# Performance work log

Measured on AMD Instinct MI355X. Metric: run time of the kernel, lower is better.

Reference implementation:

```python
import math
import jax, jax.numpy as jnp
import numpy as np

D_MODEL = 1024
N_HEAD = 16
HEAD_DIM = D_MODEL // N_HEAD
ATTN_MULT = 1.0
# standparam=False (muP): scaling = head_dim**-1 * sqrt(attn_mult)
SCALING = (1.0 / HEAD_DIM) * math.sqrt(ATTN_MULT)
EPS = 1e-5


def layernorm(x, w, b):
    mu = jnp.mean(x, axis=-1, keepdims=True)
    var = jnp.mean(jnp.square(x - mu), axis=-1, keepdims=True)
    return (x - mu) * jax.lax.rsqrt(var + EPS) * w + b


def setup_inputs() -> dict:
    key = jax.random.key(0)
    ks = jax.random.split(key, 6)
    L, N, E = 2048, 2, D_MODEL
    std = 0.02
    return {
        "x": jax.random.normal(ks[0], (L, N, E), jnp.float32),
        "ln1_w": jnp.ones((E,), jnp.float32),
        "ln1_b": jnp.zeros((E,), jnp.float32),
        "in_proj_w": jax.random.normal(ks[1], (3 * E, E), jnp.float32) * std,
        "in_proj_b": jnp.zeros((3 * E,), jnp.float32),
        "out_w": jax.random.normal(ks[2], (E, E), jnp.float32) * std,
        "out_b": jnp.zeros((E,), jnp.float32),
        "ln2_w": jnp.ones((E,), jnp.float32),
        "ln2_b": jnp.zeros((E,), jnp.float32),
        "fc_w": jax.random.normal(ks[3], (4 * E, E), jnp.float32) * std,
        "fc_b": jnp.zeros((4 * E,), jnp.float32),
        "proj_w": jax.random.normal(ks[4], (E, 4 * E), jnp.float32) * std,
        "proj_b": jnp.zeros((E,), jnp.float32),
    }


def block(x, ln1_w, ln1_b, in_proj_w, in_proj_b, out_w, out_b,
          ln2_w, ln2_b, fc_w, fc_b, proj_w, proj_b):
    L, N, E = x.shape
    H, D = N_HEAD, HEAD_DIM
    # --- self-attention on ln_1(x), seq-first layout (L, N, E) ---
    y = layernorm(x, ln1_w, ln1_b)
    qkv = jnp.einsum('lne,fe->lnf', y, in_proj_w) + in_proj_b  # (L, N, 3E)
    q, k, v = jnp.split(qkv, 3, axis=-1)
    q = q * SCALING
    # (L, N, E) -> (N, H, L, D)
    def to_heads(t):
        return t.reshape(L, N, H, D).transpose(1, 2, 0, 3)
    q, k, v = to_heads(q), to_heads(k), to_heads(v)
    scores = jnp.einsum('nhld,nhsd->nhls', q, k)           # (N, H, L, L)
    w = jax.nn.softmax(scores, axis=-1)
    o = jnp.einsum('nhls,nhsd->nhld', w, v)                # (N, H, L, D)
    o = o.transpose(2, 0, 1, 3).reshape(L, N, E)
    attn_out = jnp.einsum('lne,fe->lnf', o, out_w) + out_b
    x = x + attn_out
    # --- MLP on ln_2(x): fc -> GELU -> proj ---
    z = layernorm(x, ln2_w, ln2_b)
    h = jax.nn.gelu(jnp.einsum('lne,fe->lnf', z, fc_w) + fc_b, approximate=False)
    m = jnp.einsum('lnf,ef->lne', h, proj_w) + proj_b
    return x + m


def reference(x, ln1_w, ln1_b, in_proj_w, in_proj_b, out_w, out_b,
              ln2_w, ln2_b, fc_w, fc_b, proj_w, proj_b):
    return block(x, ln1_w, ln1_b, in_proj_w, in_proj_b, out_w, out_b,
                 ln2_w, ln2_b, fc_w, fc_b, proj_w, proj_b)
```

## Files before the change

kernel.cpp:

```cpp
#include <hip/hip_runtime.h>
#include <hip/hip_bf16.h>

typedef unsigned short u16;
typedef float v4f __attribute__((ext_vector_type(4)));
typedef __bf16 v8bf __attribute__((ext_vector_type(8)));
typedef unsigned short v4u __attribute__((ext_vector_type(4)));
typedef unsigned short v8u __attribute__((ext_vector_type(8)));

#define EMB 1024
#define TOK 4096
#define LSEQ 2048
#define NBATCH 2
#define SCALING 0.015625f
#define LN_EPS 1e-5f

__device__ __forceinline__ float bf2f(u16 u) {
  unsigned int i = ((unsigned int)u) << 16;
  return __builtin_bit_cast(float, i);
}
__device__ __forceinline__ u16 f2bf(float f) {
  __hip_bfloat16 h = __float2bfloat16(f);
  return __builtin_bit_cast(u16, h);
}
__device__ __forceinline__ v8bf load8(const u16* p) {
  return *reinterpret_cast<const v8bf*>(p);
}
__device__ __forceinline__ v4f mfma16(v8bf a, v8bf b, v4f c) {
  return __builtin_amdgcn_mfma_f32_16x16x32_bf16(a, b, c, 0, 0, 0);
}
__device__ __forceinline__ void gload16(const u16* g, u16* l) {
  __builtin_amdgcn_global_load_lds(
      (const __attribute__((address_space(1))) void*)g,
      (__attribute__((address_space(3))) void*)l, 16, 0, 0);
}
template <int N>
__device__ __forceinline__ void waitcnt_vm() {
  if constexpr (N == 0) asm volatile("s_waitcnt vmcnt(0)" ::: "memory");
  else if constexpr (N == 2) asm volatile("s_waitcnt vmcnt(2)" ::: "memory");
  else if constexpr (N == 3) asm volatile("s_waitcnt vmcnt(3)" ::: "memory");
  else if constexpr (N == 4) asm volatile("s_waitcnt vmcnt(4)" ::: "memory");
  else if constexpr (N == 6) asm volatile("s_waitcnt vmcnt(6)" ::: "memory");
  else if constexpr (N == 8) asm volatile("s_waitcnt vmcnt(8)" ::: "memory");
}
__device__ __forceinline__ float gelu_fast(float v) {
  float u = v * (0.7978845608f + 0.0356774081f * v * v);
  return v / (1.0f + __expf(-2.0f * u));
}

__global__ __launch_bounds__(256) void cvt_kernel(
    const float* __restrict__ in, u16* __restrict__ out) {
  size_t i = ((size_t)blockIdx.x * 256 + threadIdx.x) * 8;
  v4f a = *reinterpret_cast<const v4f*>(in + i);
  v4f b = *reinterpret_cast<const v4f*>(in + i + 4);
  v8u r;
#pragma unroll
  for (int j = 0; j < 4; j++) { r[j] = f2bf(a[j]); r[4 + j] = f2bf(b[j]); }
  *reinterpret_cast<v8u*>(out + i) = r;
}

__global__ __launch_bounds__(256) void addred_kernel(
    float* __restrict__ out, const u16* __restrict__ p0) {
  size_t i = ((size_t)blockIdx.x * 256 + threadIdx.x) * 8;
  v4f a0 = *reinterpret_cast<const v4f*>(out + i);
  v4f a1 = *reinterpret_cast<const v4f*>(out + i + 4);
  v8u pp = *reinterpret_cast<const v8u*>(p0 + i);
#pragma unroll
  for (int j = 0; j < 4; j++) {
    a0[j] += bf2f(pp[j]);
    a1[j] += bf2f(pp[4 + j]);
  }
  *reinterpret_cast<v4f*>(out + i) = a0;
  *reinterpret_cast<v4f*>(out + i + 4) = a1;
}

template <int MODE>
__global__ __launch_bounds__(256) void ln_kernel(
    const void* __restrict__ xin, const float* __restrict__ w,
    const float* __restrict__ b, u16* __restrict__ y) {
  int t = blockIdx.x, tid = threadIdx.x;
  float v[4];
  if (MODE == 0) {
    v4u raw = *reinterpret_cast<const v4u*>((const u16*)xin + (size_t)t * EMB + tid * 4);
#pragma unroll
    for (int j = 0; j < 4; j++) v[j] = bf2f(raw[j]);
  } else {
    v4f raw = *reinterpret_cast<const v4f*>((const float*)xin + (size_t)t * EMB + tid * 4);
#pragma unroll
    for (int j = 0; j < 4; j++) v[j] = raw[j];
  }
  float s = v[0] + v[1] + v[2] + v[3];
  float ss = v[0] * v[0] + v[1] * v[1] + v[2] * v[2] + v[3] * v[3];
#pragma unroll
  for (int off = 32; off >= 1; off >>= 1) {
    s += __shfl_xor(s, off);
    ss += __shfl_xor(ss, off);
  }
  __shared__ float sm[4], sq[4];
  if ((tid & 63) == 0) { sm[tid >> 6] = s; sq[tid >> 6] = ss; }
  __syncthreads();
  s = sm[0] + sm[1] + sm[2] + sm[3];
  ss = sq[0] + sq[1] + sq[2] + sq[3];
  float mu = s * (1.0f / EMB);
  float var = ss * (1.0f / EMB) - mu * mu;
  float rstd = rsqrtf(var + LN_EPS);
  v4f wv = *reinterpret_cast<const v4f*>(w + tid * 4);
  v4f bv = *reinterpret_cast<const v4f*>(b + tid * 4);
  v4u out;
#pragma unroll
  for (int j = 0; j < 4; j++) out[j] = f2bf((v[j] - mu) * rstd * wv[j] + bv[j]);
  *reinterpret_cast<v4u*>(y + (size_t)t * EMB + tid * 4) = out;
}

template <int BM, int BN>
__global__ __launch_bounds__(256) void gemm_db_kernel(
    const u16* __restrict__ A, const u16* __restrict__ W,
    const float* __restrict__ bias, int K, int Nout, int mode,
    u16* __restrict__ out_bf, float* __restrict__ out_f,
    const float* __restrict__ res_f32, const u16* __restrict__ res_bf) {
  constexpr int NJ = BM * BN / 4096;
  constexpr int CWV = 4 / (BM / 64);
  __shared__ alignas(16) u16 lA[2][BM * 32];
  __shared__ alignas(16) u16 lB[2][BN * 32];

  int tid = threadIdx.x;
  int lane = tid & 63, wid = tid >> 6;
  int quad = lane >> 4, l16 = lane & 15;
  int row0 = blockIdx.x * BM;
  int col0 = blockIdx.y * BN;
  int rw = (wid / CWV) * 64;
  int cw = (wid % CWV) * (BN / CWV);

  v4f zero = {0.f, 0.f, 0.f, 0.f};
  v4f acc[4][NJ];
#pragma unroll
  for (int i = 0; i < 4; i++)
#pragma unroll
    for (int j = 0; j < NJ; j++) acc[i][j] = zero;

  int wbase8 = (tid & 192) * 8;

  auto stage = [&](int buf, int k0) {
    const u16* Ab = A + (size_t)row0 * K + k0;
    const u16* Wb = W + (size_t)col0 * K + k0;
#pragma unroll
    for (int n = 0; n < BM / 64; n++) {
      int slot = n * 256 + tid;
      int seg = slot / BM, r = slot & (BM - 1);
      gload16(Ab + (size_t)r * K + seg * 8, &lA[buf][n * 2048 + wbase8]);
    }
#pragma unroll
    for (int n = 0; n < BN / 64; n++) {
      int slot = n * 256 + tid;
      int seg = slot / BN, r = slot & (BN - 1);
      gload16(Wb + (size_t)r * K + seg * 8, &lB[buf][n * 2048 + wbase8]);
    }
  };

  stage(0, 0);
  int buf = 0;
  for (int k0 = 0; k0 < K; k0 += 32) {
    __syncthreads();
    if (k0 + 32 < K) stage(buf ^ 1, k0 + 32);

    v8bf af[4], bfr[NJ];
#pragma unroll
    for (int i = 0; i < 4; i++)
      af[i] = load8(&lA[buf][(quad * BM + rw + i * 16 + l16) * 8]);
#pragma unroll
    for (int j = 0; j < NJ; j++)
      bfr[j] = load8(&lB[buf][(quad * BN + cw + j * 16 + l16) * 8]);
#pragma unroll
    for (int i = 0; i < 4; i++)
#pragma unroll
      for (int j = 0; j < NJ; j++)
        acc[i][j] = mfma16(af[i], bfr[j], acc[i][j]);
    buf ^= 1;
  }

#pragma unroll
  for (int i = 0; i < 4; i++) {
    int rbase = row0 + rw + i * 16 + quad * 4;
#pragma unroll
    for (int j = 0; j < NJ; j++) {
      int c = col0 + cw + j * 16 + l16;
      float bv = bias[c];
#pragma unroll
      for (int r = 0; r < 4; r++) {
        int tok = rbase + r;
        float v = acc[i][j][r] + bv;
        size_t idx = (size_t)tok * Nout + c;
        if (mode == 1) {
          out_bf[idx] = f2bf(res_f32[idx] + v);
        } else if (mode == 3) {
          out_f[idx] = bf2f(res_bf[idx]) + v;
        }
      }
    }
  }
}

template <int BM, int BN>
__global__ __launch_bounds__(512, 2) void gemm_big_kernel(
    const u16* __restrict__ A, const u16* __restrict__ W,
    const float* __restrict__ bias, int K, int Nout, int mode,
    u16* __restrict__ out_bf, float* __restrict__ out_f,
    const u16* __restrict__ res_bf) {
  constexpr int NI = BM / 32;
  constexpr int NJ = BN / 64;
  constexpr int LOADS = BM / 128 + BN / 128;
  __shared__ alignas(16) u16 lA[3][BM * 32];
  __shared__ alignas(16) u16 lB[3][BN * 32];

  int tid = threadIdx.x;
  int lane = tid & 63, wid = tid >> 6;
  int quad = lane >> 4, l16 = lane & 15;
  int row0 = blockIdx.x * BM;
  int col0 = blockIdx.y * BN;
  int rw = (wid >> 2) * (BM / 2);
  int cw = (wid & 3) * (BN / 4);

  int kbeg = 0, kend = K;
  if (mode == 5) {
    int half = K >> 1;
    kbeg = blockIdx.z * half;
    kend = kbeg + half;
  }
  int nt = (kend - kbeg) >> 5;

  v4f zero = {0.f, 0.f, 0.f, 0.f};
  v4f acc[NI][NJ];
#pragma unroll
  for (int i = 0; i < NI; i++)
#pragma unroll
    for (int j = 0; j < NJ; j++) acc[i][j] = zero;

  int wbase8 = (tid & 448) * 8;

  auto stage = [&](int buf, int k0) {
    const u16* Ab = A + (size_t)row0 * K + k0;
    const u16* Wb = W + (size_t)col0 * K + k0;
#pragma unroll
    for (int n = 0; n < BM / 128; n++) {
      int p = n * 512 + tid;
      int r = p >> 2, sp = p & 3;
      int sl = sp ^ ((r >> 1) & 3);
      gload16(Ab + (size_t)r * K + sl * 8, &lA[buf][n * 4096 + wbase8]);
    }
#pragma unroll
    for (int n = 0; n < BN / 128; n++) {
      int p = n * 512 + tid;
      int r = p >> 2, sp = p & 3;
      int sl = sp ^ ((r >> 1) & 3);
      gload16(Wb + (size_t)r * K + sl * 8, &lB[buf][n * 4096 + wbase8]);
    }
  };

  auto compute = [&](int bidx) {
    v8bf af[NI], bfr[NJ];
#pragma unroll
    for (int i = 0; i < NI; i++) {
      int ra = rw + i * 16 + l16;
      af[i] = load8(&lA[bidx][((ra << 2) + (quad ^ ((ra >> 1) & 3))) << 3]);
    }
#pragma unroll
    for (int j = 0; j < NJ; j++) {
      int rb = cw + j * 16 + l16;
      bfr[j] = load8(&lB[bidx][((rb << 2) + (quad ^ ((rb >> 1) & 3))) << 3]);
    }
#pragma unroll
    for (int i = 0; i < NI; i++)
#pragma unroll
      for (int j = 0; j < NJ; j++)
        acc[i][j] = mfma16(af[i], bfr[j], acc[i][j]);
  };

  stage(0, kbeg);
  stage(1, kbeg + 32);
  for (int t = 0; t < nt - 1; ++t) {
    waitcnt_vm<LOADS>();
    __builtin_amdgcn_s_barrier();
    if (t + 2 < nt) stage((t + 2) % 3, kbeg + (t + 2) * 32);
    compute(t % 3);
  }
  waitcnt_vm<0>();
  __builtin_amdgcn_s_barrier();
  compute((nt - 1) % 3);

#pragma unroll
  for (int i = 0; i < NI; i++) {
    int rbase = row0 + rw + i * 16 + quad * 4;
#pragma unroll
    for (int j = 0; j < NJ; j++) {
      int c = col0 + cw + j * 16 + l16;
      float bv = bias[c];
#pragma unroll
      for (int r = 0; r < 4; r++) {
        int tok = rbase + r;
        float raw = acc[i][j][r];
        float v = raw + bv;
        if (mode == 4) {
          int region = c >> 10;
          int cc = c & 1023;
          int hh = cc >> 6, dd = cc & 63;
          int l = tok >> 1, nn = tok & 1;
          size_t hb = (size_t)(nn * 16 + hh);
          if (region == 0) {
            out_bf[(hb * LSEQ + l) * 64 + dd] = f2bf(v * SCALING);
          } else if (region == 1) {
            out_bf[4194304 + (hb * LSEQ + l) * 64 + dd] = f2bf(v);
          } else {
            out_bf[8388608 + (hb * 64 + dd) * LSEQ + l] = f2bf(v);
          }
        } else {
          size_t idx = (size_t)tok * Nout + c;
          if (mode == 2) {
            out_bf[idx] = f2bf(gelu_fast(v));
          } else {
            if (blockIdx.z == 0) {
              out_bf[idx] = f2bf(raw);
            } else {
              out_f[idx] = v + bf2f(res_bf[idx]);
            }
          }
        }
      }
    }
  }
}

__global__ __launch_bounds__(256) void flash_kernel(
    const u16* __restrict__ qb, const u16* __restrict__ kb,
    const u16* __restrict__ vtb, u16* __restrict__ o) {
  int tid = threadIdx.x;
  int lane = tid & 63, wid = tid >> 6;
  int quad = lane >> 4, l16 = lane & 15;
  int qt = blockIdx.x;
  int nh = blockIdx.y;
  int n = nh >> 4, h = nh & 15;

  __shared__ alignas(16) u16 lK[4096];
  __shared__ alignas(16) u16 lV[4096];
  __shared__ alignas(16) u16 pl[128][72];

  const u16* khead = kb + (size_t)nh * (LSEQ * 64);
  const u16* vhead = vtb + (size_t)nh * (64 * LSEQ);

  v4f zero = {0.f, 0.f, 0.f, 0.f};
  v4f acc_o[2][4];
  float lsum[2][4];
#pragma unroll
  for (int i = 0; i < 2; i++) {
#pragma unroll
    for (int r = 0; r < 4; r++) lsum[i][r] = 0.f;
#pragma unroll
    for (int jd = 0; jd < 4; jd++) acc_o[i][jd] = zero;
  }

  v8bf qf[2][2];
#pragma unroll
  for (int i = 0; i < 2; i++) {
    int lq = qt * 128 + wid * 32 + i * 16 + l16;
#pragma unroll
    for (int kk = 0; kk < 2; kk++)
      qf[i][kk] = load8(qb + ((size_t)nh * LSEQ + lq) * 64 + kk * 32 + quad * 8);
  }

  int swl = l16 & 7;
  int srow = tid >> 3;
  int sseg0 = tid & 7;
  int lbase = (tid & 192) * 8;

  for (int s0 = 0; s0 < LSEQ; s0 += 64) {
#pragma unroll
    for (int p = 0; p < 2; p++) {
      int row = p * 32 + srow;
      int seg = sseg0 ^ (row & 7);
      gload16(khead + (size_t)(s0 + row) * 64 + seg * 8, &lK[p * 2048 + lbase]);
      gload16(vhead + (size_t)row * LSEQ + s0 + seg * 8, &lV[p * 2048 + lbase]);
    }
    __syncthreads();

    v4f sacc[2][4];
#pragma unroll
    for (int i = 0; i < 2; i++)
#pragma unroll
      for (int j = 0; j < 4; j++) sacc[i][j] = zero;
#pragma unroll
    for (int kk = 0; kk < 2; kk++) {
      v8bf kf[4];
#pragma unroll
      for (int j = 0; j < 4; j++) {
        int rl = j * 16 + l16;
        kf[j] = load8(&lK[((rl << 3) + (((kk << 2) + quad) ^ swl)) << 3]);
      }
#pragma unroll
      for (int i = 0; i < 2; i++)
#pragma unroll
        for (int j = 0; j < 4; j++)
          sacc[i][j] = mfma16(qf[i][kk], kf[j], sacc[i][j]);
    }

#pragma unroll
    for (int i = 0; i < 2; i++) {
#pragma unroll
      for (int r = 0; r < 4; r++) {
        float ps = 0.f;
#pragma unroll
        for (int j = 0; j < 4; j++) {
          float p = __expf(fminf(sacc[i][j][r], 60.f));
          ps += p;
          pl[wid * 32 + i * 16 + quad * 4 + r][j * 16 + l16] = f2bf(p);
        }
        lsum[i][r] += ps;
      }
    }

#pragma unroll
    for (int kk = 0; kk < 2; kk++) {
      v8bf pf[2], vf[4];
#pragma unroll
      for (int i = 0; i < 2; i++)
        pf[i] = load8(&pl[wid * 32 + i * 16 + l16][kk * 32 + quad * 8]);
#pragma unroll
      for (int jd = 0; jd < 4; jd++) {
        int dl = jd * 16 + l16;
        vf[jd] = load8(&lV[((dl << 3) + (((kk << 2) + quad) ^ swl)) << 3]);
      }
#pragma unroll
      for (int i = 0; i < 2; i++)
#pragma unroll
        for (int jd = 0; jd < 4; jd++)
          acc_o[i][jd] = mfma16(pf[i], vf[jd], acc_o[i][jd]);
    }
    __syncthreads();
  }

#pragma unroll
  for (int i = 0; i < 2; i++) {
#pragma unroll
    for (int r = 0; r < 4; r++) {
      float s = lsum[i][r];
#pragma unroll
      for (int off = 1; off < 16; off <<= 1) s += __shfl_xor(s, off);
      float inv = 1.0f / s;
      int lq = qt * 128 + wid * 32 + i * 16 + quad * 4 + r;
      size_t t = (size_t)lq * NBATCH + n;
#pragma unroll
      for (int jd = 0; jd < 4; jd++)
        o[t * EMB + h * 64 + jd * 16 + l16] = f2bf(acc_o[i][jd][r] * inv);
    }
  }
}

extern "C" void kernel_launch(void* const* d_in, const int* in_sizes, int n_in,
                              void* d_out, int out_size, void* d_ws,
                              size_t ws_size, hipStream_t stream) {
  const float* x = (const float*)d_in[0];
  const float* ln1_w = (const float*)d_in[1];
  const float* ln1_b = (const float*)d_in[2];
  const float* in_proj_w = (const float*)d_in[3];
  const float* in_proj_b = (const float*)d_in[4];
  const float* out_w = (const float*)d_in[5];
  const float* out_b = (const float*)d_in[6];
  const float* ln2_w = (const float*)d_in[7];
  const float* ln2_b = (const float*)d_in[8];
  const float* fc_w = (const float*)d_in[9];
  const float* fc_b = (const float*)d_in[10];
  const float* proj_w = (const float*)d_in[11];
  const float* proj_b = (const float*)d_in[12];
  float* out = (float*)d_out;

  char* ws = (char*)d_ws;
  u16* wbuf = (u16*)(ws + 0);
  u16* y = (u16*)(ws + 8388608);
  u16* qkvh = (u16*)(ws + 16777216);
  u16* o = (u16*)(ws + 8388608);
  u16* hbuf = (u16*)(ws + 8388608);
  u16* x2 = (u16*)(ws + 41943040);
  u16* z = (u16*)(ws + 50331648);

  u16* qb = qkvh;
  u16* kb = qkvh + 4194304;
  u16* vtb = qkvh + 8388608;

  ln_kernel<1><<<TOK, 256, 0, stream>>>((const void*)x, ln1_w, ln1_b, y);
  cvt_kernel<<<1536, 256, 0, stream>>>(in_proj_w, wbuf);
  gemm_big_kernel<256, 256><<<dim3(16, 12), 512, 0, stream>>>(
      y, wbuf, in_proj_b, EMB, 3 * EMB, 4, qkvh, nullptr, nullptr);
  flash_kernel<<<dim3(16, 32), 256, 0, stream>>>(qb, kb, vtb, o);
  cvt_kernel<<<512, 256, 0, stream>>>(out_w, wbuf);
  gemm_db_kernel<64, 128><<<dim3(64, 8), 256, 0, stream>>>(
      o, wbuf, out_b, EMB, EMB, 1, x2, nullptr, x, nullptr);
  ln_kernel<0><<<TOK, 256, 0, stream>>>((const void*)x2, ln2_w, ln2_b, z);
  cvt_kernel<<<2048, 256, 0, stream>>>(fc_w, wbuf);
  gemm_big_kernel<256, 256><<<dim3(16, 16), 512, 0, stream>>>(
      z, wbuf, fc_b, EMB, 4 * EMB, 2, hbuf, nullptr, nullptr);
  cvt_kernel<<<2048, 256, 0, stream>>>(proj_w, wbuf);
  gemm_big_kernel<256, 128><<<dim3(16, 8, 2), 512, 0, stream>>>(
      hbuf, wbuf, proj_b, 4 * EMB, EMB, 5, z, out, x2);
  addred_kernel<<<2048, 256, 0, stream>>>(out, z);
}
```

Before: 462.7 us.

## Restructure big GEMM into 8-wave ping-pong schedule with 64-wide K tiles

Replaces the triple-buffered 32-wide K loop with a double-buffered 64-wide K tile split into two row/column halves. Loads of the next tile are interleaved with four quarter MFMA phases, with barriers and s_setprio raising MFMA priority. The proj GEMM now uses 256x256 tiles, giving half as many blocks. The aim is to overlap global-to-LDS traffic with matrix math and cut barrier overhead per K element, at the cost of more barriers per iteration and fewer blocks for the proj GEMM.

```diff
diff --git a/kernel.cpp b/kernel.cpp
--- a/kernel.cpp
+++ b/kernel.cpp
@@ -14,6 +14,8 @@
 #define SCALING 0.015625f
 #define LN_EPS 1e-5f
 
+template <int V> struct ic { static constexpr int v = V; };
+
 __device__ __forceinline__ float bf2f(u16 u) {
   unsigned int i = ((unsigned int)u) << 16;
   return __builtin_bit_cast(float, i);
@@ -37,7 +39,6 @@
 __device__ __forceinline__ void waitcnt_vm() {
   if constexpr (N == 0) asm volatile("s_waitcnt vmcnt(0)" ::: "memory");
   else if constexpr (N == 2) asm volatile("s_waitcnt vmcnt(2)" ::: "memory");
-  else if constexpr (N == 3) asm volatile("s_waitcnt vmcnt(3)" ::: "memory");
   else if constexpr (N == 4) asm volatile("s_waitcnt vmcnt(4)" ::: "memory");
   else if constexpr (N == 6) asm volatile("s_waitcnt vmcnt(6)" ::: "memory");
   else if constexpr (N == 8) asm volatile("s_waitcnt vmcnt(8)" ::: "memory");
@@ -200,97 +201,150 @@
 }
 
 template <int BM, int BN>
-__global__ __launch_bounds__(512, 2) void gemm_big_kernel(
+__global__ __launch_bounds__(512, 2) void gemm8_kernel(
     const u16* __restrict__ A, const u16* __restrict__ W,
     const float* __restrict__ bias, int K, int Nout, int mode,
     u16* __restrict__ out_bf, float* __restrict__ out_f,
     const u16* __restrict__ res_bf) {
-  constexpr int NI = BM / 32;
-  constexpr int NJ = BN / 64;
-  constexpr int LOADS = BM / 128 + BN / 128;
-  __shared__ alignas(16) u16 lA[3][BM * 32];
-  __shared__ alignas(16) u16 lB[3][BN * 32];
+  static_assert(BM == 256 && BN == 256, "geometry fixed at 256^2");
+  __shared__ alignas(16) u16 lA[2][2][8192];
+  __shared__ alignas(16) u16 lB[2][2][8192];
 
   int tid = threadIdx.x;
   int lane = tid & 63, wid = tid >> 6;
   int quad = lane >> 4, l16 = lane & 15;
-  int row0 = blockIdx.x * BM;
-  int col0 = blockIdx.y * BN;
-  int rw = (wid >> 2) * (BM / 2);
-  int cw = (wid & 3) * (BN / 4);
+  int rwh = wid >> 2;
+  int cwq = wid & 3;
+  int row0 = blockIdx.x * BM, col0 = blockIdx.y * BN;
 
   int kbeg = 0, kend = K;
-  if (mode == 5) {
-    int half = K >> 1;
-    kbeg = blockIdx.z * half;
-    kend = kbeg + half;
-  }
-  int nt = (kend - kbeg) >> 5;
+  if (mode == 5) { int h = K >> 1; kbeg = blockIdx.z * h; kend = kbeg + h; }
+  int nt = (kend - kbeg) >> 6;
 
   v4f zero = {0.f, 0.f, 0.f, 0.f};
-  v4f acc[NI][NJ];
-#pragma unroll
-  for (int i = 0; i < NI; i++)
-#pragma unroll
-    for (int j = 0; j < NJ; j++) acc[i][j] = zero;
-
-  int wbase8 = (tid & 448) * 8;
-
-  auto stage = [&](int buf, int k0) {
-    const u16* Ab = A + (size_t)row0 * K + k0;
-    const u16* Wb = W + (size_t)col0 * K + k0;
-#pragma unroll
-    for (int n = 0; n < BM / 128; n++) {
+  v4f acc[8][4];
+#pragma unroll
+  for (int i = 0; i < 8; i++)
+#pragma unroll
+    for (int j = 0; j < 4; j++) acc[i][j] = zero;
+
+  int wslot = tid & 448;
+
+  auto stA = [&](int buf, int g, int kt) {
+    int koff = kbeg + kt * 64;
+#pragma unroll
+    for (int n = 0; n < 2; n++) {
       int p = n * 512 + tid;
-      int r = p >> 2, sp = p & 3;
-      int sl = sp ^ ((r >> 1) & 3);
-      gload16(Ab + (size_t)r * K + sl * 8, &lA[buf][n * 4096 + wbase8]);
-    }
-#pragma unroll
-    for (int n = 0; n < BN / 128; n++) {
+      int ri = p >> 3, sp = p & 7;
+      int row = ((ri >> 6) << 7) | (g << 6) | (ri & 63);
+      int sl = sp ^ (ri & 7);
+      gload16(A + (size_t)(row0 + row) * K + koff + sl * 8,
+              &lA[buf][g][(n * 512 + wslot) * 8]);
+    }
+  };
+  auto stB = [&](int buf, int g, int kt) {
+    int koff = kbeg + kt * 64;
+#pragma unroll
+    for (int n = 0; n < 2; n++) {
       int p = n * 512 + tid;
-      int r = p >> 2, sp = p & 3;
-      int sl = sp ^ ((r >> 1) & 3);
-      gload16(Wb + (size_t)r * K + sl * 8, &lB[buf][n * 4096 + wbase8]);
+      int ci = p >> 3, sp = p & 7;
+      int col = ((ci >> 5) << 6) | (g << 5) | (ci & 31);
+      int sl = sp ^ (ci & 7);
+      gload16(W + (size_t)(col0 + col) * K + koff + sl * 8,
+              &lB[buf][g][(n * 512 + wslot) * 8]);
     }
   };
 
-  auto compute = [&](int bidx) {
-    v8bf af[NI], bfr[NJ];
-#pragma unroll
-    for (int i = 0; i < NI; i++) {
-      int ra = rw + i * 16 + l16;
-      af[i] = load8(&lA[bidx][((ra << 2) + (quad ^ ((ra >> 1) & 3))) << 3]);
-    }
-#pragma unroll
-    for (int j = 0; j < NJ; j++) {
-      int rb = cw + j * 16 + l16;
-      bfr[j] = load8(&lB[bidx][((rb << 2) + (quad ^ ((rb >> 1) & 3))) << 3]);
-    }
-#pragma unroll
-    for (int i = 0; i < NI; i++)
-#pragma unroll
-      for (int j = 0; j < NJ; j++)
-        acc[i][j] = mfma16(af[i], bfr[j], acc[i][j]);
+  auto rdA = [&](v8bf (&af)[4][2], int buf, int g) {
+#pragma unroll
+    for (int i = 0; i < 4; i++) {
+      int ri = (rwh << 6) + i * 16 + l16;
+      int rs = ri * 8, rx = ri & 7;
+#pragma unroll
+      for (int kk = 0; kk < 2; kk++)
+        af[i][kk] = load8(&lA[buf][g][(rs + ((kk * 4 + quad) ^ rx)) * 8]);
+    }
   };
-
-  stage(0, kbeg);
-  stage(1, kbeg + 32);
+  auto rdB = [&](v8bf (&bf)[2][2], int buf, int g) {
+#pragma unroll
+    for (int j = 0; j < 2; j++) {
+      int ci = (cwq << 5) + j * 16 + l16;
+      int rs = ci * 8, rx = ci & 7;
+#pragma unroll
+      for (int kk = 0; kk < 2; kk++)
+        bf[j][kk] = load8(&lB[buf][g][(rs + ((kk * 4 + quad) ^ rx)) * 8]);
+    }
+  };
+  auto mm = [&](auto QA, auto QB, v8bf (&af)[4][2], v8bf (&bf)[2][2]) {
+    constexpr int qa = decltype(QA)::v, qb = decltype(QB)::v;
+#pragma unroll
+    for (int i = 0; i < 4; i++)
+#pragma unroll
+      for (int j = 0; j < 2; j++)
+#pragma unroll
+        for (int kk = 0; kk < 2; kk++)
+          acc[qa * 4 + i][qb * 2 + j] =
+              mfma16(af[i][kk], bf[j][kk], acc[qa * 4 + i][qb * 2 + j]);
+  };
+
+  v8bf af[4][2], b0[2][2], b1[2][2];
+
+  stA(0, 0, 0); stB(0, 0, 0); stB(0, 1, 0); stA(0, 1, 0);
+  waitcnt_vm<4>();
+  __builtin_amdgcn_s_barrier();
+
   for (int t = 0; t < nt - 1; ++t) {
-    waitcnt_vm<LOADS>();
-    __builtin_amdgcn_s_barrier();
-    if (t + 2 < nt) stage((t + 2) % 3, kbeg + (t + 2) * 32);
-    compute(t % 3);
+    int buf = t & 1, nb = buf ^ 1;
+    rdA(af, buf, 0); rdB(b0, buf, 0);
+    stA(nb, 0, t + 1);
+    __builtin_amdgcn_s_barrier();
+    __builtin_amdgcn_s_setprio(1);
+    mm(ic<0>{}, ic<0>{}, af, b0);
+    __builtin_amdgcn_s_setprio(0);
+    waitcnt_vm<4>();
+    __builtin_amdgcn_s_barrier();
+    rdB(b1, buf, 1);
+    stB(nb, 0, t + 1);
+    __builtin_amdgcn_s_barrier();
+    __builtin_amdgcn_s_setprio(1);
+    mm(ic<0>{}, ic<1>{}, af, b1);
+    __builtin_amdgcn_s_setprio(0);
+    waitcnt_vm<4>();
+    __builtin_amdgcn_s_barrier();
+    rdA(af, buf, 1);
+    stB(nb, 1, t + 1);
+    __builtin_amdgcn_s_barrier();
+    __builtin_amdgcn_s_setprio(1);
+    mm(ic<1>{}, ic<1>{}, af, b1);
+    __builtin_amdgcn_s_setprio(0);
+    __builtin_amdgcn_s_barrier();
+    stA(nb, 1, t + 1);
+    __builtin_amdgcn_s_barrier();
+    __builtin_amdgcn_s_setprio(1);
+    mm(ic<1>{}, ic<0>{}, af, b0);
+    __builtin_amdgcn_s_setprio(0);
+    waitcnt_vm<4>();
+    __builtin_amdgcn_s_barrier();
   }
   waitcnt_vm<0>();
   __builtin_amdgcn_s_barrier();
-  compute((nt - 1) % 3);
-
-#pragma unroll
-  for (int i = 0; i < NI; i++) {
+  {
+    int buf = (nt - 1) & 1;
+    rdA(af, buf, 0); rdB(b0, buf, 0); rdB(b1, buf, 1);
+    mm(ic<0>{}, ic<0>{}, af, b0);
+    mm(ic<0>{}, ic<1>{}, af, b1);
+    rdA(af, buf, 1);
+    mm(ic<1>{}, ic<1>{}, af, b1);
+    mm(ic<1>{}, ic<0>{}, af, b0);
+  }
+
+  int rw = rwh << 7;
+  int cw = cwq << 6;
+#pragma unroll
+  for (int i = 0; i < 8; i++) {
     int rbase = row0 + rw + i * 16 + quad * 4;
 #pragma unroll
-    for (int j = 0; j < NJ; j++) {
+    for (int j = 0; j < 4; j++) {
       int c = col0 + cw + j * 16 + l16;
       float bv = bias[c];
 #pragma unroll
@@ -485,7 +539,7 @@
 
   ln_kernel<1><<<TOK, 256, 0, stream>>>((const void*)x, ln1_w, ln1_b, y);
   cvt_kernel<<<1536, 256, 0, stream>>>(in_proj_w, wbuf);
-  gemm_big_kernel<256, 256><<<dim3(16, 12), 512, 0, stream>>>(
+  gemm8_kernel<256, 256><<<dim3(16, 12), 512, 0, stream>>>(
       y, wbuf, in_proj_b, EMB, 3 * EMB, 4, qkvh, nullptr, nullptr);
   flash_kernel<<<dim3(16, 32), 256, 0, stream>>>(qb, kb, vtb, o);
   cvt_kernel<<<512, 256, 0, stream>>>(out_w, wbuf);
@@ -493,10 +547,10 @@
       o, wbuf, out_b, EMB, EMB, 1, x2, nullptr, x, nullptr);
   ln_kernel<0><<<TOK, 256, 0, stream>>>((const void*)x2, ln2_w, ln2_b, z);
   cvt_kernel<<<2048, 256, 0, stream>>>(fc_w, wbuf);
-  gemm_big_kernel<256, 256><<<dim3(16, 16), 512, 0, stream>>>(
+  gemm8_kernel<256, 256><<<dim3(16, 16), 512, 0, stream>>>(
       z, wbuf, fc_b, EMB, 4 * EMB, 2, hbuf, nullptr, nullptr);
   cvt_kernel<<<2048, 256, 0, stream>>>(proj_w, wbuf);
-  gemm_big_kernel<256, 128><<<dim3(16, 8, 2), 512, 0, stream>>>(
+  gemm8_kernel<256, 256><<<dim3(16, 4, 2), 512, 0, stream>>>(
       hbuf, wbuf, proj_b, 4 * EMB, EMB, 5, z, out, x2);
   addred_kernel<<<2048, 256, 0, stream>>>(out, z);
 }
```

New measurement: 466.7 us. Within noise of the previous version (+0.9%).
